# Kernel tuning notes

Measured on AMD Instinct MI355X. Metric: run time of the kernel, lower is better.

## Reference

```python
import jax, jax.numpy as jnp
import numpy as np

D_MODEL = 1024
HEAD_DIM = 64
SPARSITY_RATIO = 0.1
NEG_INF = -1e9


def setup_inputs() -> dict:
    key = jax.random.key(0)
    kx, kw = jax.random.split(key)
    x = jax.random.normal(kx, (4, 4096, D_MODEL), dtype=jnp.float32)
    # nn.Linear(d_model, 3*head_dim, bias=False): weight [3*head_dim, d_model]
    W_qkv = jax.random.normal(kw, (3 * HEAD_DIM, D_MODEL), dtype=jnp.float32) / np.sqrt(D_MODEL)
    return {"x": x, "W_qkv": W_qkv}


def reference(x, W_qkv):
    B, S, _ = x.shape
    scale = HEAD_DIM ** (-0.5)
    qkv = jnp.einsum("bsd,ed->bse", x, W_qkv)  # [B,S,3*head_dim]
    q, k, v = jnp.split(qkv, 3, axis=-1)       # each [B,S,head_dim]
    scores = jnp.einsum("bqd,bkd->bqk", q, k) * scale  # [B,S,S]
    k_sparse = max(1, int(S * SPARSITY_RATIO))
    _, top_idx = jax.lax.top_k(scores, k_sparse)  # [B,S,k_sparse]
    bi = jnp.arange(B)[:, None, None]
    si = jnp.arange(S)[None, :, None]
    sparse_mask = jnp.zeros_like(scores).at[bi, si, top_idx].set(1.0)
    # attn*mask then masked_fill(mask==0, -1e9) == where(mask>0, attn, -1e9)
    masked = jnp.where(sparse_mask == 0, NEG_INF, scores * sparse_mask)
    probs = jax.nn.softmax(masked, axis=-1)
    return jnp.einsum("bqk,bkd->bqd", probs, v)
```

## Files before the change

kernel.cpp:

```cpp
#include <hip/hip_runtime.h>
#include <math.h>

#define BATCH 4
#define SEQ 4096
#define DMODEL 1024
#define HD 64
#define EE 192
#define KSP 409
#define SCALE 0.125f
#define LISTCAP 512
#define INV2048 (1.0f/2048.0f)

using half8 = __attribute__((ext_vector_type(8))) _Float16;
using half4 = __attribute__((ext_vector_type(4))) _Float16;
using f32x4 = __attribute__((ext_vector_type(4))) float;

__device__ __forceinline__ unsigned int fkey(float f) {
    unsigned int u = __float_as_uint(f);
    return (u & 0x80000000u) ? ~u : (u | 0x80000000u);
}
__device__ __forceinline__ float ikey(unsigned int k) {
    unsigned int u = (k & 0x80000000u) ? (k ^ 0x80000000u) : ~k;
    return __uint_as_float(u);
}

__global__ __launch_bounds__(256) void wsplit_kernel(const float* __restrict__ W,
                                                     _Float16* __restrict__ Whi,
                                                     _Float16* __restrict__ Wlo) {
    int i = blockIdx.x * 1024 + threadIdx.x * 4;
    float4 w = *(const float4*)&W[i];
    float f[4] = {w.x, w.y, w.z, w.w};
    half4 hv, lv;
    #pragma unroll
    for (int j = 0; j < 4; ++j) {
        _Float16 h = (_Float16)f[j];
        hv[j] = h;
        lv[j] = (_Float16)((f[j] - (float)h) * 2048.0f);
    }
    *(half4*)&Whi[i] = hv;
    *(half4*)&Wlo[i] = lv;
}

#define AH_OFF 0
#define AL_OFF 4096
#define BH_OFF 8192
#define BL_OFF 14336

__global__ __launch_bounds__(256) void qkv_mfma_kernel(const float* __restrict__ X,
        const _Float16* __restrict__ Whi, const _Float16* __restrict__ Wlo,
        _Float16* __restrict__ QH, _Float16* __restrict__ QL,
        _Float16* __restrict__ KH, _Float16* __restrict__ KL,
        float* __restrict__ V) {
    __shared__ __align__(16) unsigned char lds[20480];
    const int t = threadIdx.x;
    const int lane = t & 63;
    const int wv = t >> 6;
    const int wr = wv >> 1, wc = wv & 1;
    const int m0 = blockIdx.x * 64;
    const int n0 = blockIdx.y * 96;

    const int ar = t >> 2;
    const int akc = (t & 3) * 8;
    const int aw_addr = ((ar * 64 + (t & 3) * 16) ^ ((ar & 7) << 4));
    const int br0 = t >> 2;
    const int bw0 = ((br0 * 64 + (t & 3) * 16) ^ ((br0 & 7) << 4));
    const int br1 = 64 + (t >> 2);
    const int bw1 = ((br1 * 64 + (t & 3) * 16) ^ ((br1 & 7) << 4));

    float4 xa, xb;
    uint4 pbh0, pbl0, pbh1, pbl1;

    #define LOADG(K0) { \
        const float* xp = X + (size_t)(m0 + ar) * DMODEL + (K0) + akc; \
        xa = *(const float4*)xp; xb = *(const float4*)(xp + 4); \
        size_t wo0 = (size_t)(n0 + br0) * DMODEL + (K0) + akc; \
        pbh0 = *(const uint4*)(Whi + wo0); pbl0 = *(const uint4*)(Wlo + wo0); \
        if (t < 128) { \
            size_t wo1 = (size_t)(n0 + br1) * DMODEL + (K0) + akc; \
            pbh1 = *(const uint4*)(Whi + wo1); pbl1 = *(const uint4*)(Wlo + wo1); \
        } }

    #define WRITE_LDS() { \
        float f[8] = {xa.x, xa.y, xa.z, xa.w, xb.x, xb.y, xb.z, xb.w}; \
        half8 hv, lv; \
        _Pragma("unroll") \
        for (int i2 = 0; i2 < 8; ++i2) { \
            _Float16 h = (_Float16)f[i2]; \
            hv[i2] = h; \
            lv[i2] = (_Float16)((f[i2] - (float)h) * 2048.0f); \
        } \
        *(half8*)(lds + AH_OFF + aw_addr) = hv; \
        *(half8*)(lds + AL_OFF + aw_addr) = lv; \
        *(uint4*)(lds + BH_OFF + bw0) = pbh0; \
        *(uint4*)(lds + BL_OFF + bw0) = pbl0; \
        if (t < 128) { \
            *(uint4*)(lds + BH_OFF + bw1) = pbh1; \
            *(uint4*)(lds + BL_OFF + bw1) = pbl1; \
        } }

    f32x4 hh[2][3], xx[2][3];
    #pragma unroll
    for (int mi = 0; mi < 2; ++mi)
        #pragma unroll
        for (int ni = 0; ni < 3; ++ni) {
            hh[mi][ni] = (f32x4){0.f, 0.f, 0.f, 0.f};
            xx[mi][ni] = (f32x4){0.f, 0.f, 0.f, 0.f};
        }

    LOADG(0);
    WRITE_LDS();
    __syncthreads();

    const int kb = (lane >> 4) << 4;

    for (int it = 0; it < 32; ++it) {
        if (it < 31) LOADG((it + 1) * 32);

        half8 ah[2], al[2], bh[3], bl[3];
        #pragma unroll
        for (int mi = 0; mi < 2; ++mi) {
            int ra = wr * 32 + mi * 16 + (lane & 15);
            int ad = ((ra * 64 + kb) ^ ((ra & 7) << 4));
            ah[mi] = *(const half8*)(lds + AH_OFF + ad);
            al[mi] = *(const half8*)(lds + AL_OFF + ad);
        }
        #pragma unroll
        for (int ni = 0; ni < 3; ++ni) {
            int rb = wc * 48 + ni * 16 + (lane & 15);
            int bd = ((rb * 64 + kb) ^ ((rb & 7) << 4));
            bh[ni] = *(const half8*)(lds + BH_OFF + bd);
            bl[ni] = *(const half8*)(lds + BL_OFF + bd);
        }
        #pragma unroll
        for (int mi = 0; mi < 2; ++mi)
            #pragma unroll
            for (int ni = 0; ni < 3; ++ni) {
                hh[mi][ni] = __builtin_amdgcn_mfma_f32_16x16x32_f16(ah[mi], bh[ni], hh[mi][ni], 0, 0, 0);
                xx[mi][ni] = __builtin_amdgcn_mfma_f32_16x16x32_f16(ah[mi], bl[ni], xx[mi][ni], 0, 0, 0);
                xx[mi][ni] = __builtin_amdgcn_mfma_f32_16x16x32_f16(al[mi], bh[ni], xx[mi][ni], 0, 0, 0);
            }
        __syncthreads();
        if (it < 31) { WRITE_LDS(); __syncthreads(); }
    }

    #pragma unroll
    for (int mi = 0; mi < 2; ++mi)
        #pragma unroll
        for (int ni = 0; ni < 3; ++ni) {
            int col = n0 + wc * 48 + ni * 16 + (lane & 15);
            int rowb = m0 + wr * 32 + mi * 16 + ((lane >> 4) << 2);
            #pragma unroll
            for (int j = 0; j < 4; ++j) {
                float val = hh[mi][ni][j] + xx[mi][ni][j] * INV2048;
                int row = rowb + j;
                if (col < 64) {
                    _Float16 h = (_Float16)val;
                    QH[(size_t)row * HD + col] = h;
                    QL[(size_t)row * HD + col] = (_Float16)((val - (float)h) * 2048.0f);
                } else if (col < 128) {
                    _Float16 h = (_Float16)val;
                    KH[(size_t)row * HD + (col - 64)] = h;
                    KL[(size_t)row * HD + (col - 64)] = (_Float16)((val - (float)h) * 2048.0f);
                } else {
                    V[(size_t)row * HD + (col - 128)] = val;
                }
            }
        }
}

#define SQH_OFF 0
#define SQL_OFF 16384
#define SKH_OFF 32768
#define SKL_OFF 40960

__global__ __launch_bounds__(256) void scores_mfma_kernel(
        const _Float16* __restrict__ QH, const _Float16* __restrict__ QL,
        const _Float16* __restrict__ KH, const _Float16* __restrict__ KL,
        float* __restrict__ Sc) {
    __shared__ __align__(16) unsigned char lds[49152];
    const int t = threadIdx.x;
    const int lane = t & 63;
    const int wv = t >> 6;
    const int i0 = blockIdx.y * 128;
    const int j0 = blockIdx.x * 64;

    #pragma unroll
    for (int u = 0; u < 4; ++u) {
        int ch = t + 256 * u;
        int r = ch >> 3;
        int kbyte = (ch & 7) * 16;
        int ad = (r * 128 + kbyte) ^ ((r & 7) << 4);
        *(uint4*)(lds + SQH_OFF + ad) = *(const uint4*)((const char*)QH + (size_t)(i0 + r) * 128 + kbyte);
        *(uint4*)(lds + SQL_OFF + ad) = *(const uint4*)((const char*)QL + (size_t)(i0 + r) * 128 + kbyte);
    }
    #pragma unroll
    for (int u = 0; u < 2; ++u) {
        int ch = t + 256 * u;
        int r = ch >> 3;
        int kbyte = (ch & 7) * 16;
        int ad = (r * 128 + kbyte) ^ ((r & 7) << 4);
        *(uint4*)(lds + SKH_OFF + ad) = *(const uint4*)((const char*)KH + (size_t)(j0 + r) * 128 + kbyte);
        *(uint4*)(lds + SKL_OFF + ad) = *(const uint4*)((const char*)KL + (size_t)(j0 + r) * 128 + kbyte);
    }
    __syncthreads();

    f32x4 hh[2][4], xx[2][4];
    #pragma unroll
    for (int mi = 0; mi < 2; ++mi)
        #pragma unroll
        for (int ni = 0; ni < 4; ++ni) {
            hh[mi][ni] = (f32x4){0.f, 0.f, 0.f, 0.f};
            xx[mi][ni] = (f32x4){0.f, 0.f, 0.f, 0.f};
        }

    #pragma unroll
    for (int ks = 0; ks < 2; ++ks) {
        int kbyte = ks * 64 + ((lane >> 4) << 4);
        half8 qh[2], ql[2], kh[4], kl[4];
        #pragma unroll
        for (int mi = 0; mi < 2; ++mi) {
            int r = wv * 32 + mi * 16 + (lane & 15);
            int ad = (r * 128 + kbyte) ^ ((r & 7) << 4);
            qh[mi] = *(const half8*)(lds + SQH_OFF + ad);
            ql[mi] = *(const half8*)(lds + SQL_OFF + ad);
        }
        #pragma unroll
        for (int ni = 0; ni < 4; ++ni) {
            int r = ni * 16 + (lane & 15);
            int ad = (r * 128 + kbyte) ^ ((r & 7) << 4);
            kh[ni] = *(const half8*)(lds + SKH_OFF + ad);
            kl[ni] = *(const half8*)(lds + SKL_OFF + ad);
        }
        #pragma unroll
        for (int mi = 0; mi < 2; ++mi)
            #pragma unroll
            for (int ni = 0; ni < 4; ++ni) {
                hh[mi][ni] = __builtin_amdgcn_mfma_f32_16x16x32_f16(qh[mi], kh[ni], hh[mi][ni], 0, 0, 0);
                xx[mi][ni] = __builtin_amdgcn_mfma_f32_16x16x32_f16(qh[mi], kl[ni], xx[mi][ni], 0, 0, 0);
                xx[mi][ni] = __builtin_amdgcn_mfma_f32_16x16x32_f16(ql[mi], kh[ni], xx[mi][ni], 0, 0, 0);
            }
    }

    #pragma unroll
    for (int mi = 0; mi < 2; ++mi)
        #pragma unroll
        for (int ni = 0; ni < 4; ++ni) {
            int col = j0 + ni * 16 + (lane & 15);
            int rowb = i0 + wv * 32 + mi * 16 + ((lane >> 4) << 2);
            #pragma unroll
            for (int j = 0; j < 4; ++j) {
                float s = SCALE * (hh[mi][ni][j] + xx[mi][ni][j] * INV2048);
                Sc[(size_t)(rowb + j) * SEQ + col] = s;
            }
        }
}

__global__ __launch_bounds__(256) void topk_attn_kernel(const float* __restrict__ V,
                                                        const float* __restrict__ Sc,
                                                        float* __restrict__ Out, int b) {
    __shared__ unsigned int hist[4][256];
    __shared__ unsigned int wsum[4];
    __shared__ unsigned int swin[2];
    __shared__ unsigned int smax[4];
    __shared__ float sredf[4];
    __shared__ uint2 lw[LISTCAP];
    __shared__ float pvred[4][4][64];
    __shared__ float sZ;

    const int t = threadIdx.x;
    const int lane = t & 63;
    const int wv = t >> 6;
    const unsigned long long ltmask = (1ull << lane) - 1ull;

    const float* row = Sc + (size_t)blockIdx.x * SEQ;
    unsigned int key[16];
    #pragma unroll
    for (int u = 0; u < 4; ++u) {
        float4 v4 = *(const float4*)&row[u * 1024 + t * 4];
        key[u * 4 + 0] = fkey(v4.x);
        key[u * 4 + 1] = fkey(v4.y);
        key[u * 4 + 2] = fkey(v4.z);
        key[u * 4 + 3] = fkey(v4.w);
    }

    unsigned int prefix = 0;
    int remain = KSP;
    for (int shift = 24; shift >= 0; shift -= 8) {
        #pragma unroll
        for (int i = 0; i < 4; ++i) ((unsigned int*)hist)[t + 256 * i] = 0;
        __syncthreads();
        #pragma unroll
        for (int su = 0; su < 16; ++su) {
            unsigned int k = key[su];
            bool ok = (shift == 24) || (((k ^ prefix) >> (shift + 8)) == 0);
            if (ok) atomicAdd(&hist[wv][(k >> shift) & 255], 1u);
        }
        __syncthreads();
        unsigned int c = hist[0][255 - t] + hist[1][255 - t] + hist[2][255 - t] + hist[3][255 - t];
        unsigned int s = c;
        #pragma unroll
        for (int off = 1; off < 64; off <<= 1) {
            unsigned int o = __shfl_up(s, off);
            if (lane >= off) s += o;
        }
        if (lane == 63) wsum[wv] = s;
        __syncthreads();
        unsigned int base = 0;
        for (int w2 = 0; w2 < wv; ++w2) base += wsum[w2];
        s += base;
        unsigned int cgt = s - c;
        if (s >= (unsigned)remain && cgt < (unsigned)remain) {
            swin[0] = 255u - (unsigned)t;
            swin[1] = cgt;
        }
        __syncthreads();
        prefix |= swin[0] << shift;
        remain -= (int)swin[1];
        __syncthreads();
    }
    const unsigned int thrk = prefix;

    unsigned int mk = 0;
    #pragma unroll
    for (int su = 0; su < 16; ++su) mk = max(mk, key[su]);
    #pragma unroll
    for (int off = 32; off >= 1; off >>= 1) mk = max(mk, (unsigned int)__shfl_xor(mk, off));
    if (lane == 0) smax[wv] = mk;
    __syncthreads();
    const float m = ikey(max(max(smax[0], smax[1]), max(smax[2], smax[3])));

    unsigned long long msk[16];
    unsigned int wt = 0;
    #pragma unroll
    for (int su = 0; su < 16; ++su) {
        msk[su] = __ballot(key[su] >= thrk);
        wt += (unsigned int)__popcll(msk[su]);
    }
    if (lane == 0) wsum[wv] = wt;
    __syncthreads();
    unsigned int wbase = 0;
    for (int w2 = 0; w2 < wv; ++w2) wbase += wsum[w2];
    const unsigned int total = wsum[0] + wsum[1] + wsum[2] + wsum[3];

    unsigned int pos = wbase;
    float lsum = 0.0f;
    #pragma unroll
    for (int su = 0; su < 16; ++su) {
        if (key[su] >= thrk) {
            unsigned int myoff = pos + (unsigned int)__popcll(msk[su] & ltmask);
            float s = ikey(key[su]);
            float w = __expf(s - m);
            if (myoff < LISTCAP) {
                lw[myoff] = make_uint2((unsigned)((su >> 2) * 1024 + t * 4 + (su & 3)),
                                       __float_as_uint(w));
            }
            lsum += w;
        }
        pos += (unsigned int)__popcll(msk[su]);
    }
    #pragma unroll
    for (int off = 32; off >= 1; off >>= 1) lsum += __shfl_xor(lsum, off);
    if (lane == 0) sredf[wv] = lsum;
    __syncthreads();
    if (t == 0) sZ = sredf[0] + sredf[1] + sredf[2] + sredf[3];
    __syncthreads();
    const float Zinv = 1.0f / sZ;

    const int q = lane & 15;
    const int g = lane >> 4;
    const int cc = (int)(total < LISTCAP ? total : LISTCAP);
    const float* vbase = V + (size_t)b * SEQ * HD + 4 * q;
    float a0 = 0.f, a1 = 0.f, a2 = 0.f, a3 = 0.f;
    #pragma unroll 2
    for (int n = wv * 4 + g; n < cc; n += 16) {
        uint2 e = lw[n];
        float w = __uint_as_float(e.y);
        float4 v4 = *(const float4*)(vbase + (size_t)e.x * HD);
        a0 = fmaf(w, v4.x, a0);
        a1 = fmaf(w, v4.y, a1);
        a2 = fmaf(w, v4.z, a2);
        a3 = fmaf(w, v4.w, a3);
    }
    pvred[wv][g][4 * q + 0] = a0;
    pvred[wv][g][4 * q + 1] = a1;
    pvred[wv][g][4 * q + 2] = a2;
    pvred[wv][g][4 * q + 3] = a3;
    __syncthreads();
    if (t < 64) {
        float o = 0.f;
        #pragma unroll
        for (int w2 = 0; w2 < 4; ++w2)
            #pragma unroll
            for (int g2 = 0; g2 < 4; ++g2)
                o += pvred[w2][g2][t];
        Out[((size_t)b * SEQ + blockIdx.x) * HD + t] = o * Zinv;
    }
}

extern "C" void kernel_launch(void* const* d_in, const int* in_sizes, int n_in,
                              void* d_out, int out_size, void* d_ws, size_t ws_size,
                              hipStream_t stream) {
    (void)in_sizes; (void)n_in; (void)out_size; (void)ws_size;
    const float* X = (const float*)d_in[0];
    const float* W = (const float*)d_in[1];
    float* Out = (float*)d_out;

    char* ws = (char*)d_ws;
    const size_t V_BYTES  = (size_t)BATCH * SEQ * HD * 4;
    const size_t SC_BYTES = (size_t)SEQ * SEQ * 4;
    const size_t WH_BYTES = (size_t)EE * DMODEL * 2;
    const size_t QH_BYTES = (size_t)BATCH * SEQ * HD * 2;

    float*    Vv  = (float*)(ws);
    float*    sc  = (float*)(ws + V_BYTES);
    _Float16* Whi = (_Float16*)(ws + V_BYTES + SC_BYTES);
    _Float16* Wlo = (_Float16*)(ws + V_BYTES + SC_BYTES + WH_BYTES);
    _Float16* QH  = (_Float16*)(ws + V_BYTES + SC_BYTES + 2 * WH_BYTES);
    _Float16* QL  = (_Float16*)(ws + V_BYTES + SC_BYTES + 2 * WH_BYTES + QH_BYTES);
    _Float16* KH  = (_Float16*)(ws + V_BYTES + SC_BYTES + 2 * WH_BYTES + 2 * QH_BYTES);
    _Float16* KL  = (_Float16*)(ws + V_BYTES + SC_BYTES + 2 * WH_BYTES + 3 * QH_BYTES);

    wsplit_kernel<<<EE, 256, 0, stream>>>(W, Whi, Wlo);
    qkv_mfma_kernel<<<dim3(256, 2), 256, 0, stream>>>(X, Whi, Wlo, QH, QL, KH, KL, Vv);
    for (int b = 0; b < BATCH; ++b) {
        scores_mfma_kernel<<<dim3(64, 32), 256, 0, stream>>>(
            QH + (size_t)b * SEQ * HD, QL + (size_t)b * SEQ * HD,
            KH + (size_t)b * SEQ * HD, KL + (size_t)b * SEQ * HD, sc);
        topk_attn_kernel<<<SEQ, 256, 0, stream>>>(Vv, sc, Out, b);
    }
}
```

Before: 315.2 us.

## Use 12-bit radix passes with candidate-list rank fallback for top-k threshold

The radix select that finds the top-k threshold now uses a 4096-bin histogram with 12-bit digits (12/12/8) in place of four 8-bit passes. Once the winning bin holds few enough keys (at most 512), those keys are compacted into shared memory and the exact threshold is found by brute-force ranking, so the remaining passes and their barriers are skipped. Shared memory is reused across the histogram, candidate list, weight list and PV reduction buffers, which needs an extra barrier. The larger histogram costs more zeroing and scanning per pass, and the fallback does O(cwin) work per candidate thread.

```diff
diff --git a/kernel.cpp b/kernel.cpp
--- a/kernel.cpp
+++ b/kernel.cpp
@@ -9,6 +9,7 @@
 #define KSP 409
 #define SCALE 0.125f
 #define LISTCAP 512
+#define CANDCAP 512
 #define INV2048 (1.0f/2048.0f)
 
 using half8 = __attribute__((ext_vector_type(8))) _Float16;
@@ -258,14 +259,17 @@
 __global__ __launch_bounds__(256) void topk_attn_kernel(const float* __restrict__ V,
                                                         const float* __restrict__ Sc,
                                                         float* __restrict__ Out, int b) {
-    __shared__ unsigned int hist[4][256];
+    __shared__ __align__(16) unsigned int hist[4096];
     __shared__ unsigned int wsum[4];
-    __shared__ unsigned int swin[2];
+    __shared__ unsigned int swin[3];
     __shared__ unsigned int smax[4];
     __shared__ float sredf[4];
-    __shared__ uint2 lw[LISTCAP];
-    __shared__ float pvred[4][4][64];
+    __shared__ unsigned int sthr;
     __shared__ float sZ;
+
+    unsigned int* cand = hist;
+    uint2* lw = (uint2*)(hist + 512);
+    float* pvred = (float*)(hist + 1536);
 
     const int t = threadIdx.x;
     const int lane = t & 63;
@@ -283,42 +287,110 @@
         key[u * 4 + 3] = fkey(v4.w);
     }
 
-    unsigned int prefix = 0;
+    unsigned int pfx = 0;
+    int plen = 0;
     int remain = KSP;
-    for (int shift = 24; shift >= 0; shift -= 8) {
-        #pragma unroll
-        for (int i = 0; i < 4; ++i) ((unsigned int*)hist)[t + 256 * i] = 0;
+    for (int pass = 0; pass < 3; ++pass) {
+        {
+            uint4 z = {0u, 0u, 0u, 0u};
+            #pragma unroll
+            for (int c4 = 0; c4 < 4; ++c4) *(uint4*)&hist[16 * t + 4 * c4] = z;
+        }
         __syncthreads();
         #pragma unroll
         for (int su = 0; su < 16; ++su) {
             unsigned int k = key[su];
-            bool ok = (shift == 24) || (((k ^ prefix) >> (shift + 8)) == 0);
-            if (ok) atomicAdd(&hist[wv][(k >> shift) & 255], 1u);
+            bool ok = (pass == 0) || ((k >> (32 - plen)) == pfx);
+            unsigned int dig = (pass == 0) ? (k >> 20)
+                             : (pass == 1) ? ((k >> 8) & 0xFFFu)
+                                           : (k & 0xFFu);
+            if (ok) atomicAdd(&hist[dig], 1u);
         }
         __syncthreads();
-        unsigned int c = hist[0][255 - t] + hist[1][255 - t] + hist[2][255 - t] + hist[3][255 - t];
-        unsigned int s = c;
+        unsigned int h[16];
+        #pragma unroll
+        for (int c4 = 0; c4 < 4; ++c4) {
+            uint4 h4 = *(const uint4*)&hist[16 * t + 4 * c4];
+            h[4 * c4 + 0] = h4.x; h[4 * c4 + 1] = h4.y;
+            h[4 * c4 + 2] = h4.z; h[4 * c4 + 3] = h4.w;
+        }
+        unsigned int partial = 0;
+        #pragma unroll
+        for (int i = 0; i < 16; ++i) partial += h[i];
+        unsigned int incl = partial;
         #pragma unroll
         for (int off = 1; off < 64; off <<= 1) {
-            unsigned int o = __shfl_up(s, off);
-            if (lane >= off) s += o;
-        }
-        if (lane == 63) wsum[wv] = s;
+            unsigned int o = __shfl_up(incl, off);
+            if (lane >= off) incl += o;
+        }
+        if (lane == 63) wsum[wv] = incl;
         __syncthreads();
-        unsigned int base = 0;
-        for (int w2 = 0; w2 < wv; ++w2) base += wsum[w2];
-        s += base;
-        unsigned int cgt = s - c;
-        if (s >= (unsigned)remain && cgt < (unsigned)remain) {
-            swin[0] = 255u - (unsigned)t;
-            swin[1] = cgt;
+        unsigned int wb = 0;
+        for (int w2 = 0; w2 < wv; ++w2) wb += wsum[w2];
+        const unsigned int T = wsum[0] + wsum[1] + wsum[2] + wsum[3];
+        unsigned int cum = wb + incl - partial;
+        #pragma unroll
+        for (int i = 0; i < 16; ++i) {
+            unsigned int cg = T - cum - h[i];
+            if (cg < (unsigned)remain && cg + h[i] >= (unsigned)remain) {
+                swin[0] = 16u * (unsigned)t + (unsigned)i;
+                swin[1] = cg;
+                swin[2] = h[i];
+            }
+            cum += h[i];
         }
         __syncthreads();
-        prefix |= swin[0] << shift;
+        const unsigned int dwin = swin[0];
+        const unsigned int cwin = swin[2];
         remain -= (int)swin[1];
+        const int width = (pass == 2) ? 8 : 12;
+        pfx = (pfx << width) | dwin;
+        plen += width;
         __syncthreads();
-    }
-    const unsigned int thrk = prefix;
+
+        if (pass == 2) {
+            if (t == 0) sthr = pfx;
+            break;
+        }
+        if (cwin <= CANDCAP) {
+            unsigned int wt = 0;
+            unsigned long long cm[16];
+            #pragma unroll
+            for (int su = 0; su < 16; ++su) {
+                cm[su] = __ballot((key[su] >> (32 - plen)) == pfx);
+                wt += (unsigned int)__popcll(cm[su]);
+            }
+            if (lane == 0) wsum[wv] = wt;
+            __syncthreads();
+            unsigned int pos = 0;
+            for (int w2 = 0; w2 < wv; ++w2) pos += wsum[w2];
+            #pragma unroll
+            for (int su = 0; su < 16; ++su) {
+                if ((key[su] >> (32 - plen)) == pfx) {
+                    unsigned int off = pos + (unsigned int)__popcll(cm[su] & ltmask);
+                    if (off < CANDCAP) cand[off] = key[su];
+                }
+                pos += (unsigned int)__popcll(cm[su]);
+            }
+            __syncthreads();
+            #pragma unroll
+            for (int su = 0; su < 16; ++su) {
+                unsigned int v = key[su];
+                if ((v >> (32 - plen)) == pfx) {
+                    unsigned int g = 0, e = 0;
+                    for (unsigned int j = 0; j < cwin; ++j) {
+                        unsigned int u = cand[j];
+                        g += (u > v) ? 1u : 0u;
+                        e += (u == v) ? 1u : 0u;
+                    }
+                    if (g < (unsigned)remain && g + e >= (unsigned)remain) sthr = v;
+                }
+            }
+            break;
+        }
+    }
+    __syncthreads();
+    const unsigned int thrk = sthr;
 
     unsigned int mk = 0;
     #pragma unroll
@@ -381,10 +453,11 @@
         a2 = fmaf(w, v4.z, a2);
         a3 = fmaf(w, v4.w, a3);
     }
-    pvred[wv][g][4 * q + 0] = a0;
-    pvred[wv][g][4 * q + 1] = a1;
-    pvred[wv][g][4 * q + 2] = a2;
-    pvred[wv][g][4 * q + 3] = a3;
+    __syncthreads();
+    pvred[wv * 256 + g * 64 + 4 * q + 0] = a0;
+    pvred[wv * 256 + g * 64 + 4 * q + 1] = a1;
+    pvred[wv * 256 + g * 64 + 4 * q + 2] = a2;
+    pvred[wv * 256 + g * 64 + 4 * q + 3] = a3;
     __syncthreads();
     if (t < 64) {
         float o = 0.f;
@@ -392,7 +465,7 @@
         for (int w2 = 0; w2 < 4; ++w2)
             #pragma unroll
             for (int g2 = 0; g2 < 4; ++g2)
-                o += pvred[w2][g2][t];
+                o += pvred[w2 * 256 + g2 * 64 + t];
         Out[((size_t)b * SEQ + blockIdx.x) * HD + t] = o * Zinv;
     }
 }
```

Result: slower. 815.4 us (+158.7%).

## Replace radix-histogram top-k threshold with statistics-guided bisection search

Applied to the files above, without the earlier changes.

The per-row top-k threshold search swaps the 4-pass 8-bit radix histogram, with its shared-memory atomics and prefix scans, for a bisection over the key space. The initial bracket comes from the row mean and standard deviation, assuming roughly Gaussian scores, and each step counts keys with warp shuffles and double-buffered cross-wave sums. The max reduction is folded into the first load pass and one barrier is removed from the softmax normalizer. Bisection can take up to about 32 barrier-separated iterations when the statistical bracket misses, so the cost depends on how the data is distributed.

```diff
diff --git a/kernel.cpp b/kernel.cpp
--- a/kernel.cpp
+++ b/kernel.cpp
@@ -258,14 +258,14 @@
 __global__ __launch_bounds__(256) void topk_attn_kernel(const float* __restrict__ V,
                                                         const float* __restrict__ Sc,
                                                         float* __restrict__ Out, int b) {
-    __shared__ unsigned int hist[4][256];
-    __shared__ unsigned int wsum[4];
-    __shared__ unsigned int swin[2];
-    __shared__ unsigned int smax[4];
-    __shared__ float sredf[4];
     __shared__ uint2 lw[LISTCAP];
-    __shared__ float pvred[4][4][64];
-    __shared__ float sZ;
+    __shared__ float pvred[1024];
+    __shared__ unsigned int wredA[4];
+    __shared__ unsigned int wredB[4];
+    __shared__ unsigned int wsumC[4];
+    __shared__ float fred0[4];
+    __shared__ float fred1[4];
+    __shared__ unsigned int smax4[4];
 
     const int t = threadIdx.x;
     const int lane = t & 63;
@@ -274,60 +274,77 @@
 
     const float* row = Sc + (size_t)blockIdx.x * SEQ;
     unsigned int key[16];
+    float fsum = 0.0f, fss = 0.0f;
+    unsigned int mk = 0;
     #pragma unroll
     for (int u = 0; u < 4; ++u) {
         float4 v4 = *(const float4*)&row[u * 1024 + t * 4];
-        key[u * 4 + 0] = fkey(v4.x);
-        key[u * 4 + 1] = fkey(v4.y);
-        key[u * 4 + 2] = fkey(v4.z);
-        key[u * 4 + 3] = fkey(v4.w);
-    }
-
-    unsigned int prefix = 0;
-    int remain = KSP;
-    for (int shift = 24; shift >= 0; shift -= 8) {
-        #pragma unroll
-        for (int i = 0; i < 4; ++i) ((unsigned int*)hist)[t + 256 * i] = 0;
+        float f[4] = {v4.x, v4.y, v4.z, v4.w};
+        #pragma unroll
+        for (int c = 0; c < 4; ++c) {
+            unsigned int k = fkey(f[c]);
+            key[u * 4 + c] = k;
+            mk = max(mk, k);
+            fsum += f[c];
+            fss = fmaf(f[c], f[c], fss);
+        }
+    }
+    #pragma unroll
+    for (int off = 32; off >= 1; off >>= 1) {
+        fsum += __shfl_xor(fsum, off);
+        fss  += __shfl_xor(fss, off);
+        mk = max(mk, (unsigned int)__shfl_xor(mk, off));
+    }
+    if (lane == 0) { fred0[wv] = fsum; fred1[wv] = fss; smax4[wv] = mk; }
+    __syncthreads();
+    const float mu = (fred0[0] + fred0[1] + fred0[2] + fred0[3]) * (1.0f / 4096.0f);
+    const float ms = (fred1[0] + fred1[1] + fred1[2] + fred1[3]) * (1.0f / 4096.0f);
+    const float sg = sqrtf(fmaxf(ms - mu * mu, 0.0f));
+    const float m = ikey(max(max(smax4[0], smax4[1]), max(smax4[2], smax4[3])));
+
+    const unsigned int lo0 = fkey(mu + 0.9f * sg);
+    const unsigned int hi0 = fkey(mu + 1.7f * sg);
+    unsigned int pk = 0;
+    #pragma unroll
+    for (int su = 0; su < 16; ++su) {
+        pk += (key[su] > lo0) ? 0x10000u : 0u;
+        pk += (key[su] > hi0) ? 1u : 0u;
+    }
+    #pragma unroll
+    for (int off = 32; off >= 1; off >>= 1) pk += __shfl_xor(pk, off);
+    if (lane == 0) wredA[wv] = pk;
+    __syncthreads();
+    pk = wredA[0] + wredA[1] + wredA[2] + wredA[3];
+    const unsigned int clo = pk >> 16;
+    const unsigned int chi = pk & 0xFFFFu;
+
+    unsigned int lo = 0u, hi = 0xFFFFFFFFu;
+    if (clo >= (unsigned)KSP) lo = lo0 + 1u;
+    if (chi <  (unsigned)KSP) hi = hi0;
+
+    unsigned int thrk = 0;
+    bool early = false;
+    int par = 1;
+    while (lo < hi) {
+        const unsigned int mid = lo + ((hi - lo) >> 1);
+        unsigned int c = 0;
+        #pragma unroll
+        for (int su = 0; su < 16; ++su) c += (key[su] > mid) ? 1u : 0u;
+        #pragma unroll
+        for (int off = 32; off >= 1; off >>= 1) c += __shfl_xor(c, off);
+        unsigned int* buf = par ? wredB : wredA;
+        if (lane == 0) buf[wv] = c;
         __syncthreads();
-        #pragma unroll
-        for (int su = 0; su < 16; ++su) {
-            unsigned int k = key[su];
-            bool ok = (shift == 24) || (((k ^ prefix) >> (shift + 8)) == 0);
-            if (ok) atomicAdd(&hist[wv][(k >> shift) & 255], 1u);
-        }
-        __syncthreads();
-        unsigned int c = hist[0][255 - t] + hist[1][255 - t] + hist[2][255 - t] + hist[3][255 - t];
-        unsigned int s = c;
-        #pragma unroll
-        for (int off = 1; off < 64; off <<= 1) {
-            unsigned int o = __shfl_up(s, off);
-            if (lane >= off) s += o;
-        }
-        if (lane == 63) wsum[wv] = s;
-        __syncthreads();
-        unsigned int base = 0;
-        for (int w2 = 0; w2 < wv; ++w2) base += wsum[w2];
-        s += base;
-        unsigned int cgt = s - c;
-        if (s >= (unsigned)remain && cgt < (unsigned)remain) {
-            swin[0] = 255u - (unsigned)t;
-            swin[1] = cgt;
-        }
-        __syncthreads();
-        prefix |= swin[0] << shift;
-        remain -= (int)swin[1];
-        __syncthreads();
-    }
-    const unsigned int thrk = prefix;
-
-    unsigned int mk = 0;
-    #pragma unroll
-    for (int su = 0; su < 16; ++su) mk = max(mk, key[su]);
-    #pragma unroll
-    for (int off = 32; off >= 1; off >>= 1) mk = max(mk, (unsigned int)__shfl_xor(mk, off));
-    if (lane == 0) smax[wv] = mk;
-    __syncthreads();
-    const float m = ikey(max(max(smax[0], smax[1]), max(smax[2], smax[3])));
+        c = buf[0] + buf[1] + buf[2] + buf[3];
+        par ^= 1;
+        if (c >= (unsigned)KSP) {
+            if (c == (unsigned)KSP) { thrk = mid + 1u; early = true; break; }
+            lo = mid + 1u;
+        } else {
+            hi = mid;
+        }
+    }
+    if (!early) thrk = lo;
 
     unsigned long long msk[16];
     unsigned int wt = 0;
@@ -336,11 +353,11 @@
         msk[su] = __ballot(key[su] >= thrk);
         wt += (unsigned int)__popcll(msk[su]);
     }
-    if (lane == 0) wsum[wv] = wt;
+    if (lane == 0) wsumC[wv] = wt;
     __syncthreads();
     unsigned int wbase = 0;
-    for (int w2 = 0; w2 < wv; ++w2) wbase += wsum[w2];
-    const unsigned int total = wsum[0] + wsum[1] + wsum[2] + wsum[3];
+    for (int w2 = 0; w2 < wv; ++w2) wbase += wsumC[w2];
+    const unsigned int total = wsumC[0] + wsumC[1] + wsumC[2] + wsumC[3];
 
     unsigned int pos = wbase;
     float lsum = 0.0f;
@@ -360,11 +377,9 @@
     }
     #pragma unroll
     for (int off = 32; off >= 1; off >>= 1) lsum += __shfl_xor(lsum, off);
-    if (lane == 0) sredf[wv] = lsum;
-    __syncthreads();
-    if (t == 0) sZ = sredf[0] + sredf[1] + sredf[2] + sredf[3];
-    __syncthreads();
-    const float Zinv = 1.0f / sZ;
+    if (lane == 0) fred0[wv] = lsum;
+    __syncthreads();
+    const float Zinv = 1.0f / (fred0[0] + fred0[1] + fred0[2] + fred0[3]);
 
     const int q = lane & 15;
     const int g = lane >> 4;
@@ -381,10 +396,10 @@
         a2 = fmaf(w, v4.z, a2);
         a3 = fmaf(w, v4.w, a3);
     }
-    pvred[wv][g][4 * q + 0] = a0;
-    pvred[wv][g][4 * q + 1] = a1;
-    pvred[wv][g][4 * q + 2] = a2;
-    pvred[wv][g][4 * q + 3] = a3;
+    pvred[wv * 256 + g * 64 + 4 * q + 0] = a0;
+    pvred[wv * 256 + g * 64 + 4 * q + 1] = a1;
+    pvred[wv * 256 + g * 64 + 4 * q + 2] = a2;
+    pvred[wv * 256 + g * 64 + 4 * q + 3] = a3;
     __syncthreads();
     if (t < 64) {
         float o = 0.f;
@@ -392,7 +407,7 @@
         for (int w2 = 0; w2 < 4; ++w2)
             #pragma unroll
             for (int g2 = 0; g2 < 4; ++g2)
-                o += pvred[w2][g2][t];
+                o += pvred[w2 * 256 + g2 * 64 + t];
         Out[((size_t)b * SEQ + blockIdx.x) * HD + t] = o * Zinv;
     }
 }
```

Result: faster. 295.4 us (-6.3%).
